# Optimization experiments

Hardware: AMD Instinct MI355X
Metric: run time of the kernel (lower is better)

## Reference

```python
import jax, jax.numpy as jnp
import numpy as np

N_NODES = 20000
DIM = 512
N_EDGES = 320000  # first N_NODES edges are self-loops so every node has a predecessor
EPS = 1e-7


def _logmap0(y):
    # Poincare ball (c=1) log map at origin: artanh(||y||) * y / ||y||
    n = jnp.linalg.norm(y, axis=-1, keepdims=True)
    nc = jnp.clip(n, EPS, 1.0 - 1e-6)
    return jnp.arctanh(nc) * y / nc


def _expmap0(v):
    # Poincare ball (c=1) exp map at origin: tanh(||v||) * v / ||v||
    n = jnp.linalg.norm(v, axis=-1, keepdims=True)
    nc = jnp.maximum(n, EPS)
    return jnp.tanh(nc) * v / nc


def setup_inputs() -> dict:
    key = jax.random.key(0)
    ks = jax.random.split(key, 9)
    x_raw = jax.random.normal(ks[0], (N_NODES, DIM), dtype=jnp.float32)
    nrm = jnp.linalg.norm(x_raw, axis=-1, keepdims=True)
    x = 0.7 * x_raw / (1.0 + nrm)  # strictly inside the unit ball

    rng = np.random.RandomState(0)
    src_rand = rng.randint(0, N_NODES, size=N_EDGES - N_NODES)
    dst_rand = rng.randint(0, N_NODES, size=N_EDGES - N_NODES)
    loop = np.arange(N_NODES)
    src = jnp.asarray(np.concatenate([loop, src_rand]), dtype=jnp.int32)
    dst = jnp.asarray(np.concatenate([loop, dst_rand]), dtype=jnp.int32)

    s = 1.0 / np.sqrt(DIM)
    Wq = jax.random.normal(ks[1], (DIM, DIM), jnp.float32) * s
    bq = jax.random.normal(ks[2], (DIM,), jnp.float32) * 0.01
    Wk = jax.random.normal(ks[3], (DIM, DIM), jnp.float32) * s
    bk = jax.random.normal(ks[4], (DIM,), jnp.float32) * 0.01
    Wv = jax.random.normal(ks[5], (DIM, DIM), jnp.float32) * s
    bv = jax.random.normal(ks[6], (DIM,), jnp.float32) * 0.01
    Wo = jax.random.normal(ks[7], (DIM, DIM), jnp.float32) * s
    bo = jax.random.normal(ks[8], (DIM,), jnp.float32) * 0.01
    return dict(x=x, src=src, dst=dst, Wq=Wq, bq=bq, Wk=Wk, bk=bk,
                Wv=Wv, bv=bv, Wo=Wo, bo=bo)


def reference(x, src, dst, Wq, bq, Wk, bk, Wv, bv, Wo, bo):
    n_nodes, d = x.shape
    scale = 1.0 / jnp.sqrt(jnp.asarray(d, x.dtype))

    t = _logmap0(x)                                  # [N, d] tangent vectors
    q = (t @ Wq.T + bq) * scale                      # torch MHA scales q
    k = t @ Wk.T + bk
    v = t @ Wv.T + bv

    # Per-destination attention over predecessor (src) neighbors.
    scores = jnp.sum(q[dst] * k[src], axis=-1)       # [E]
    m = jax.ops.segment_max(scores, dst, num_segments=n_nodes)
    e = jnp.exp(scores - m[dst])
    denom = jax.ops.segment_sum(e, dst, num_segments=n_nodes)
    alpha = e / denom[dst]                           # [E] softmax weights

    attn = jax.ops.segment_sum(alpha[:, None] * v[src], dst,
                               num_segments=n_nodes)  # [N, d]
    new_h = attn @ Wo.T + bo                          # MHA output projection
    return _expmap0(new_h)
```

## Files before the change

kernel.cpp:

```cpp
#include <hip/hip_runtime.h>
#include <math.h>
#include <stdint.h>

#define NND 20000
#define DIMK 512
#define NE  320000

typedef __attribute__((ext_vector_type(8))) short short8;
typedef __attribute__((ext_vector_type(4))) float floatx4;
typedef __attribute__((ext_vector_type(2))) float float2v;

__device__ inline float bf2f(unsigned short h) {
    unsigned int u = ((unsigned int)h) << 16;
    return __uint_as_float(u);
}
__device__ inline unsigned short f2bf(float f) {
    unsigned int u = __float_as_uint(f);
    unsigned int r = (u + 0x7fffu + ((u >> 16) & 1u)) >> 16;
    return (unsigned short)r;
}
__device__ __forceinline__ float2v bfpair(unsigned int u) {
    float2v r;
    r.x = __uint_as_float(u << 16);
    r.y = __uint_as_float(u & 0xffff0000u);
    return r;
}

__device__ __forceinline__ void gld_lds16(const unsigned short* g, unsigned short* l) {
    __builtin_amdgcn_global_load_lds(
        (const __attribute__((address_space(1))) void*)g,
        (__attribute__((address_space(3))) void*)l,
        16, 0, 0);
}

__global__ __launch_bounds__(256) void k_pre(const float* __restrict__ x,
                                             const float* __restrict__ Wq,
                                             const float* __restrict__ Wk,
                                             const float* __restrict__ Wv,
                                             const float* __restrict__ Wo,
                                             const float* __restrict__ bq,
                                             const float* __restrict__ bk,
                                             const float* __restrict__ bv,
                                             unsigned short* __restrict__ t,
                                             unsigned short* __restrict__ Wqkv,
                                             unsigned short* __restrict__ Wob,
                                             float* __restrict__ biasf,
                                             float scale_q) {
    int blk = blockIdx.x, tid = threadIdx.x;
    if (blk < 5000) {
        int row = blk * 4 + (tid >> 6);
        int lane = tid & 63;
        const floatx4* xp = (const floatx4*)(x + (size_t)row * DIMK + lane * 8);
        floatx4 x0 = xp[0], x1 = xp[1];
        float ss = 0.f;
#pragma unroll
        for (int i = 0; i < 4; i++) { ss += x0[i] * x0[i]; ss += x1[i] * x1[i]; }
#pragma unroll
        for (int off = 32; off >= 1; off >>= 1) ss += __shfl_xor(ss, off, 64);
        float n  = sqrtf(ss);
        float nc = fminf(fmaxf(n, 1e-7f), 1.0f - 1e-6f);
        float fac = atanhf(nc) / nc;
        union { short8 v; unsigned short u[8]; } o;
#pragma unroll
        for (int i = 0; i < 4; i++) { o.u[i] = f2bf(fac * x0[i]); o.u[4 + i] = f2bf(fac * x1[i]); }
        *(short8*)(t + (size_t)row * DIMK + lane * 8) = o.v;
    } else if (blk < 6024) {
        int i = (blk - 5000) * 256 + tid;
        int m = i >> 16, j = i & 65535;
        const float* in; unsigned short* out; float sc = 1.0f;
        if (m == 0)      { in = Wq; out = Wqkv;               sc = scale_q; }
        else if (m == 1) { in = Wk; out = Wqkv + 512 * DIMK;  sc = 16.0f; }
        else if (m == 2) { in = Wv; out = Wqkv + 1024 * DIMK; }
        else             { in = Wo; out = Wob; }
        floatx4 f = *(const floatx4*)(in + (size_t)j * 4);
        union { unsigned long long d; unsigned short u[4]; } o;
#pragma unroll
        for (int q = 0; q < 4; q++) o.u[q] = f2bf(f[q] * sc);
        *(unsigned long long*)(out + (size_t)j * 4) = o.d;
    } else {
        int i = (blk - 6024) * 256 + tid;
        if (i < 512) biasf[i] = bq[i] * scale_q;
        else if (i < 1024) biasf[i] = bk[i - 512] * 16.0f;
        else if (i < 1536) biasf[i] = bv[i - 1024];
    }
}

__global__ __launch_bounds__(256) void k_gemm(const unsigned short* __restrict__ A,
                                              const unsigned short* __restrict__ B,
                                              const float* __restrict__ biasf,
                                              unsigned short* __restrict__ out_q,
                                              unsigned char*  __restrict__ out_k8,
                                              unsigned short* __restrict__ out_v,
                                              float* __restrict__ out_f,
                                              int M, int MT, int NT, int Ncols) {
    __shared__ unsigned short smem[16384];
    int b = blockIdx.x;
    int xcd = b & 7, i = b >> 3;
    int nt = i % NT, mt = (i / NT) * 8 + xcd;
    if (mt >= MT) return;
    int m0 = mt * 128, n0 = nt * 128;
    int tid = threadIdx.x, wv = tid >> 6, ln = tid & 63;
    int lr = ln & 15, qd = ln >> 4;
    int mh = wv >> 1, nh = wv & 1;

    floatx4 acc[4][4] = {};
    int srow = wv * 16 + (ln >> 2);
    int scol = (ln & 3) * 8;

    {
        unsigned short* Ab = smem;
        unsigned short* Bb = smem + 8192;
#pragma unroll
        for (int p = 0; p < 2; p++) {
            int tr = p * 64 + srow;
            int ar = m0 + tr; if (ar > M - 1) ar = M - 1;
            gld_lds16(A + (size_t)ar * DIMK + scol, Ab + (p * 64 + wv * 16) * 32);
            gld_lds16(B + (size_t)(n0 + tr) * DIMK + scol, Bb + (p * 64 + wv * 16) * 32);
        }
    }

    for (int it = 0; it < 16; it++) {
        int cur = it & 1, nxt = cur ^ 1;
        __syncthreads();
        if (it + 1 < 16) {
            int kb = (it + 1) * 32;
            unsigned short* Ab = smem + nxt * 4096;
            unsigned short* Bb = smem + 8192 + nxt * 4096;
#pragma unroll
            for (int p = 0; p < 2; p++) {
                int tr = p * 64 + srow;
                int ar = m0 + tr; if (ar > M - 1) ar = M - 1;
                gld_lds16(A + (size_t)ar * DIMK + kb + scol, Ab + (p * 64 + wv * 16) * 32);
                gld_lds16(B + (size_t)(n0 + tr) * DIMK + kb + scol, Bb + (p * 64 + wv * 16) * 32);
            }
        }
        const unsigned short* Ac = smem + cur * 4096;
        const unsigned short* Bc = smem + 8192 + cur * 4096;
        short8 af[4], bfr[4];
#pragma unroll
        for (int mi = 0; mi < 4; mi++)
            af[mi] = *(const short8*)(Ac + (mh * 64 + mi * 16 + lr) * 32 + qd * 8);
#pragma unroll
        for (int ni = 0; ni < 4; ni++)
            bfr[ni] = *(const short8*)(Bc + (nh * 64 + ni * 16 + lr) * 32 + qd * 8);
#pragma unroll
        for (int mi = 0; mi < 4; mi++)
#pragma unroll
            for (int ni = 0; ni < 4; ni++)
                acc[mi][ni] = __builtin_amdgcn_mfma_f32_16x16x32_bf16(af[mi], bfr[ni], acc[mi][ni], 0, 0, 0);
    }

    float bb[4];
#pragma unroll
    for (int ni = 0; ni < 4; ni++) bb[ni] = biasf[n0 + nh * 64 + ni * 16 + lr];

    if (!out_f) {
        int region = nt >> 2;
        int col0 = (nt & 3) * 128;
        unsigned short* cs = smem;
#pragma unroll
        for (int g = 0; g < 4; g++) {
            __syncthreads();
            if (mh == (g >> 1)) {
                int miB = (g & 1) * 2;
#pragma unroll
                for (int m2 = 0; m2 < 2; m2++) {
                    int mi = miB + m2;
                    int lrow = mi * 16 + qd * 4 - (g & 1) * 32;
#pragma unroll
                    for (int ni = 0; ni < 4; ni++) {
                        int col = nh * 64 + ni * 16 + lr;
#pragma unroll
                        for (int r = 0; r < 4; r++)
                            cs[(lrow + r) * 128 + col] = f2bf(acc[mi][ni][r] + bb[ni]);
                    }
                }
            }
            __syncthreads();
#pragma unroll
            for (int itr = 0; itr < 2; itr++) {
                int slot = itr * 256 + tid;
                int row = slot >> 4, cg = slot & 15;
                int gm = m0 + g * 32 + row;
                if (gm < M) {
                    short8 vv = *(const short8*)(cs + row * 128 + cg * 8);
                    if (region == 1) {
                        union { short8 v; unsigned short u[8]; } pk; pk.v = vv;
                        int w0 = 0, w1 = 0;
                        w0 = __builtin_amdgcn_cvt_pk_fp8_f32(bf2f(pk.u[0]), bf2f(pk.u[1]), w0, false);
                        w0 = __builtin_amdgcn_cvt_pk_fp8_f32(bf2f(pk.u[2]), bf2f(pk.u[3]), w0, true);
                        w1 = __builtin_amdgcn_cvt_pk_fp8_f32(bf2f(pk.u[4]), bf2f(pk.u[5]), w1, false);
                        w1 = __builtin_amdgcn_cvt_pk_fp8_f32(bf2f(pk.u[6]), bf2f(pk.u[7]), w1, true);
                        uint2 o; o.x = (unsigned int)w0; o.y = (unsigned int)w1;
                        *(uint2*)(out_k8 + (size_t)gm * 512 + col0 + cg * 8) = o;
                    } else {
                        unsigned short* dp = (region == 0) ? out_q : out_v;
                        *(short8*)(dp + (size_t)gm * 512 + col0 + cg * 8) = vv;
                    }
                }
            }
        }
    } else {
#pragma unroll
        for (int ni = 0; ni < 4; ni++) {
            int gn = n0 + nh * 64 + ni * 16 + lr;
#pragma unroll
            for (int mi = 0; mi < 4; mi++) {
                int gm0 = m0 + mh * 64 + mi * 16 + qd * 4;
#pragma unroll
                for (int r = 0; r < 4; r++) {
                    int gm = gm0 + r;
                    if (gm < M) out_f[(size_t)gm * Ncols + gn] = acc[mi][ni][r] + bb[ni];
                }
            }
        }
    }
}

__global__ void k_hist(const int* __restrict__ dst, int* __restrict__ counts) {
    int e = blockIdx.x * 256 + threadIdx.x;
    if (e < NE) atomicAdd(&counts[dst[e]], 1);
}

__global__ __launch_bounds__(1024) void k_scan(const int* __restrict__ counts,
                                               int* __restrict__ offsets,
                                               int* __restrict__ pos) {
    const int C = 20;
    __shared__ int wsum[16];
    __shared__ int wpre[16];
    int tid = threadIdx.x, lane = tid & 63, w = tid >> 6;
    int local[C];
    int run = 0;
#pragma unroll
    for (int i = 0; i < C; i++) {
        int idx = tid * C + i;
        int c = (idx < NND) ? counts[idx] : 0;
        local[i] = run; run += c;
    }
    int v = run;
#pragma unroll
    for (int off = 1; off < 64; off <<= 1) {
        int u = __shfl_up(v, off, 64);
        if (lane >= off) v += u;
    }
    if (lane == 63) wsum[w] = v;
    __syncthreads();
    if (tid == 0) { int acc = 0; for (int i = 0; i < 16; i++) { wpre[i] = acc; acc += wsum[i]; } }
    __syncthreads();
    int texcl = wpre[w] + (v - run);
#pragma unroll
    for (int i = 0; i < C; i++) {
        int idx = tid * C + i;
        if (idx < NND) { int o = texcl + local[i]; offsets[idx] = o; pos[idx] = o; }
    }
    if (tid == 1023) offsets[NND] = texcl + run;
}

__global__ void k_scatter(const int* __restrict__ dst, const int* __restrict__ src,
                          int* __restrict__ pos, int* __restrict__ ssrc) {
    int e = blockIdx.x * 256 + threadIdx.x;
    if (e < NE) { int p = atomicAdd(&pos[dst[e]], 1); ssrc[p] = src[e]; }
}

__global__ __launch_bounds__(256) void k_fsa(const int* __restrict__ offsets,
                                             const int* __restrict__ ssrc,
                                             const unsigned short* __restrict__ qb,
                                             const unsigned char* __restrict__ kf8,
                                             const unsigned short* __restrict__ vb,
                                             unsigned short* __restrict__ attn) {
    __shared__ float sacc[4][512];
    __shared__ float sden[4];
    int n = blockIdx.x, tid = threadIdx.x, wv = tid >> 6, ln = tid & 63;
    int beg = offsets[n], end = offsets[n + 1];
    union { short8 v; unsigned short u[8]; } qu;
    qu.v = *(const short8*)(qb + (size_t)n * 512 + ln * 8);
    float2v qf2[4];
#pragma unroll
    for (int j = 0; j < 4; j++) {
        qf2[j].x = bf2f(qu.u[2 * j]);
        qf2[j].y = bf2f(qu.u[2 * j + 1]);
    }
    float2v av2[4] = {{0,0},{0,0},{0,0},{0,0}};
    float den = 0.f;
    int i = beg + wv * 2;
    for (; i + 1 < end; i += 8) {
        int s0 = ssrc[i], s1 = ssrc[i + 1];
        uint2 kd0 = *(const uint2*)(kf8 + (size_t)s0 * 512 + ln * 8);
        uint2 kd1 = *(const uint2*)(kf8 + (size_t)s1 * 512 + ln * 8);
        float2v a0 = {0, 0}, a1 = {0, 0};
        float2v p;
        p = __builtin_amdgcn_cvt_pk_f32_fp8(kd0.x, false); a0 += qf2[0] * p;
        p = __builtin_amdgcn_cvt_pk_f32_fp8(kd0.x, true);  a0 += qf2[1] * p;
        p = __builtin_amdgcn_cvt_pk_f32_fp8(kd0.y, false); a0 += qf2[2] * p;
        p = __builtin_amdgcn_cvt_pk_f32_fp8(kd0.y, true);  a0 += qf2[3] * p;
        p = __builtin_amdgcn_cvt_pk_f32_fp8(kd1.x, false); a1 += qf2[0] * p;
        p = __builtin_amdgcn_cvt_pk_f32_fp8(kd1.x, true);  a1 += qf2[1] * p;
        p = __builtin_amdgcn_cvt_pk_f32_fp8(kd1.y, false); a1 += qf2[2] * p;
        p = __builtin_amdgcn_cvt_pk_f32_fp8(kd1.y, true);  a1 += qf2[3] * p;
        float d0 = a0.x + a0.y, d1 = a1.x + a1.y;
#pragma unroll
        for (int off = 32; off >= 1; off >>= 1) {
            d0 += __shfl_xor(d0, off, 64);
            d1 += __shfl_xor(d1, off, 64);
        }
        float w0 = __expf(d0), w1 = __expf(d1);
        den += w0 + w1;
        uint4 vd0 = *(const uint4*)(vb + (size_t)s0 * 512 + ln * 8);
        uint4 vd1 = *(const uint4*)(vb + (size_t)s1 * 512 + ln * 8);
        float2v w20 = {w0, w0}, w21 = {w1, w1};
        av2[0] += w20 * bfpair(vd0.x); av2[0] += w21 * bfpair(vd1.x);
        av2[1] += w20 * bfpair(vd0.y); av2[1] += w21 * bfpair(vd1.y);
        av2[2] += w20 * bfpair(vd0.z); av2[2] += w21 * bfpair(vd1.z);
        av2[3] += w20 * bfpair(vd0.w); av2[3] += w21 * bfpair(vd1.w);
    }
    if (i < end) {
        int s0 = ssrc[i];
        uint2 kd0 = *(const uint2*)(kf8 + (size_t)s0 * 512 + ln * 8);
        float2v a0 = {0, 0};
        float2v p;
        p = __builtin_amdgcn_cvt_pk_f32_fp8(kd0.x, false); a0 += qf2[0] * p;
        p = __builtin_amdgcn_cvt_pk_f32_fp8(kd0.x, true);  a0 += qf2[1] * p;
        p = __builtin_amdgcn_cvt_pk_f32_fp8(kd0.y, false); a0 += qf2[2] * p;
        p = __builtin_amdgcn_cvt_pk_f32_fp8(kd0.y, true);  a0 += qf2[3] * p;
        float d0 = a0.x + a0.y;
#pragma unroll
        for (int off = 32; off >= 1; off >>= 1) d0 += __shfl_xor(d0, off, 64);
        float w0 = __expf(d0);
        den += w0;
        uint4 vd0 = *(const uint4*)(vb + (size_t)s0 * 512 + ln * 8);
        float2v w20 = {w0, w0};
        av2[0] += w20 * bfpair(vd0.x);
        av2[1] += w20 * bfpair(vd0.y);
        av2[2] += w20 * bfpair(vd0.z);
        av2[3] += w20 * bfpair(vd0.w);
    }
    floatx4 s0v = {av2[0].x, av2[0].y, av2[1].x, av2[1].y};
    floatx4 s1v = {av2[2].x, av2[2].y, av2[3].x, av2[3].y};
    *(floatx4*)&sacc[wv][ln * 8]     = s0v;
    *(floatx4*)&sacc[wv][ln * 8 + 4] = s1v;
    if (ln == 0) sden[wv] = den;
    __syncthreads();
    float inv = 1.0f / (sden[0] + sden[1] + sden[2] + sden[3]);
    int c = tid * 2;
    float t0 = sacc[0][c] + sacc[1][c] + sacc[2][c] + sacc[3][c];
    float t1 = sacc[0][c + 1] + sacc[1][c + 1] + sacc[2][c + 1] + sacc[3][c + 1];
    attn[(size_t)n * 512 + c]     = f2bf(t0 * inv);
    attn[(size_t)n * 512 + c + 1] = f2bf(t1 * inv);
}

__global__ __launch_bounds__(64) void k_expmap(float* h) {
    int row = blockIdx.x, lane = threadIdx.x;
    floatx4* hp = (floatx4*)(h + (size_t)row * DIMK + lane * 8);
    floatx4 h0 = hp[0], h1 = hp[1];
    float ss = 0.f;
#pragma unroll
    for (int i = 0; i < 4; i++) { ss += h0[i] * h0[i]; ss += h1[i] * h1[i]; }
#pragma unroll
    for (int off = 32; off >= 1; off >>= 1) ss += __shfl_xor(ss, off, 64);
    float n  = sqrtf(ss);
    float nc = fmaxf(n, 1e-7f);
    float fac = tanhf(nc) / nc;
#pragma unroll
    for (int i = 0; i < 4; i++) { h0[i] *= fac; h1[i] *= fac; }
    hp[0] = h0; hp[1] = h1;
}

extern "C" void kernel_launch(void* const* d_in, const int* in_sizes, int n_in,
                              void* d_out, int out_size, void* d_ws, size_t ws_size,
                              hipStream_t stream) {
    const float* x  = (const float*)d_in[0];
    const int* src  = (const int*)d_in[1];
    const int* dst  = (const int*)d_in[2];
    const float* Wq = (const float*)d_in[3];
    const float* bq = (const float*)d_in[4];
    const float* Wk = (const float*)d_in[5];
    const float* bk = (const float*)d_in[6];
    const float* Wv = (const float*)d_in[7];
    const float* bv = (const float*)d_in[8];
    const float* Wo = (const float*)d_in[9];
    const float* bo = (const float*)d_in[10];
    float* out = (float*)d_out;

    char* ws = (char*)d_ws;
    const size_t RB = (size_t)NND * DIMK * 2;
    const size_t KB8 = (size_t)NND * DIMK;
    const size_t WB = (size_t)DIMK * DIMK * 2;
    unsigned short* t    = (unsigned short*)(ws);
    unsigned short* qb   = (unsigned short*)(ws + RB);
    unsigned short* vb   = (unsigned short*)(ws + 2 * RB);
    unsigned char*  kf8  = (unsigned char*)(ws + 3 * RB);
    unsigned short* Wqkv = (unsigned short*)(ws + 3 * RB + KB8);
    unsigned short* Wob  = (unsigned short*)(ws + 3 * RB + KB8 + 3 * WB);
    float* biasf         = (float*)(ws + 3 * RB + KB8 + 4 * WB);
    char* p = ws + 3 * RB + KB8 + 4 * WB + 1536 * 4;
    int* ssrc    = (int*)p;
    int* counts  = ssrc + NE;
    int* offsets = counts + NND;
    int* pos     = offsets + NND + 2;
    unsigned short* attn = t;

    hipMemsetAsync(counts, 0, (size_t)NND * 4, stream);

    const float scale_q = 0.04419417382415922f / 16.0f;
    k_pre<<<6030, 256, 0, stream>>>(x, Wq, Wk, Wv, Wo, bq, bk, bv,
                                    t, Wqkv, Wob, biasf, scale_q);

    k_hist<<<(NE + 255) / 256, 256, 0, stream>>>(dst, counts);
    k_scan<<<1, 1024, 0, stream>>>(counts, offsets, pos);
    k_scatter<<<(NE + 255) / 256, 256, 0, stream>>>(dst, src, pos, ssrc);

    k_gemm<<<8 * 20 * 12, 256, 0, stream>>>(t, Wqkv, biasf, qb, kf8, vb, nullptr,
                                            NND, 157, 12, 1536);

    k_fsa<<<NND, 256, 0, stream>>>(offsets, ssrc, qb, kf8, vb, attn);

    k_gemm<<<8 * 20 * 4, 256, 0, stream>>>(attn, Wob, bo, nullptr, nullptr, nullptr, out,
                                           NND, 157, 4, 512);
    k_expmap<<<NND, 64, 0, stream>>>(out);
}
```

Baseline: 312.4 us.

## Store V as FP8 interleaved with K and fold histogram into prep kernel

V is now scaled by 16 and stored in FP8 next to K in one interleaved 1024-byte row per node, so each gathered neighbor's K and V come from a single row. This halves V gather traffic in the attention kernel and improves locality. The 16x scale is undone in the softmax normalisation. The degree histogram is merged into the preprocessing kernel to remove one launch. The cost is lower V precision, with FP8 rounding error in the output.

```diff
diff --git a/kernel.cpp b/kernel.cpp
--- a/kernel.cpp
+++ b/kernel.cpp
@@ -18,12 +18,6 @@
     unsigned int u = __float_as_uint(f);
     unsigned int r = (u + 0x7fffu + ((u >> 16) & 1u)) >> 16;
     return (unsigned short)r;
-}
-__device__ __forceinline__ float2v bfpair(unsigned int u) {
-    float2v r;
-    r.x = __uint_as_float(u << 16);
-    r.y = __uint_as_float(u & 0xffff0000u);
-    return r;
 }
 
 __device__ __forceinline__ void gld_lds16(const unsigned short* g, unsigned short* l) {
@@ -41,6 +35,8 @@
                                              const float* __restrict__ bq,
                                              const float* __restrict__ bk,
                                              const float* __restrict__ bv,
+                                             const int* __restrict__ dst,
+                                             int* __restrict__ counts,
                                              unsigned short* __restrict__ t,
                                              unsigned short* __restrict__ Wqkv,
                                              unsigned short* __restrict__ Wob,
@@ -70,18 +66,21 @@
         const float* in; unsigned short* out; float sc = 1.0f;
         if (m == 0)      { in = Wq; out = Wqkv;               sc = scale_q; }
         else if (m == 1) { in = Wk; out = Wqkv + 512 * DIMK;  sc = 16.0f; }
-        else if (m == 2) { in = Wv; out = Wqkv + 1024 * DIMK; }
+        else if (m == 2) { in = Wv; out = Wqkv + 1024 * DIMK; sc = 16.0f; }
         else             { in = Wo; out = Wob; }
         floatx4 f = *(const floatx4*)(in + (size_t)j * 4);
         union { unsigned long long d; unsigned short u[4]; } o;
 #pragma unroll
         for (int q = 0; q < 4; q++) o.u[q] = f2bf(f[q] * sc);
         *(unsigned long long*)(out + (size_t)j * 4) = o.d;
-    } else {
+    } else if (blk < 6030) {
         int i = (blk - 6024) * 256 + tid;
         if (i < 512) biasf[i] = bq[i] * scale_q;
         else if (i < 1024) biasf[i] = bk[i - 512] * 16.0f;
-        else if (i < 1536) biasf[i] = bv[i - 1024];
+        else if (i < 1536) biasf[i] = bv[i - 1024] * 16.0f;
+    } else {
+        int e = (blk - 6030) * 256 + tid;
+        if (e < NE) atomicAdd(&counts[dst[e]], 1);
     }
 }
 
@@ -89,8 +88,7 @@
                                               const unsigned short* __restrict__ B,
                                               const float* __restrict__ biasf,
                                               unsigned short* __restrict__ out_q,
-                                              unsigned char*  __restrict__ out_k8,
-                                              unsigned short* __restrict__ out_v,
+                                              unsigned char*  __restrict__ out_kv8,
                                               float* __restrict__ out_f,
                                               int M, int MT, int NT, int Ncols) {
     __shared__ unsigned short smem[16384];
@@ -184,7 +182,9 @@
                 int gm = m0 + g * 32 + row;
                 if (gm < M) {
                     short8 vv = *(const short8*)(cs + row * 128 + cg * 8);
-                    if (region == 1) {
+                    if (region == 0) {
+                        *(short8*)(out_q + (size_t)gm * 512 + col0 + cg * 8) = vv;
+                    } else {
                         union { short8 v; unsigned short u[8]; } pk; pk.v = vv;
                         int w0 = 0, w1 = 0;
                         w0 = __builtin_amdgcn_cvt_pk_fp8_f32(bf2f(pk.u[0]), bf2f(pk.u[1]), w0, false);
@@ -192,10 +192,8 @@
                         w1 = __builtin_amdgcn_cvt_pk_fp8_f32(bf2f(pk.u[4]), bf2f(pk.u[5]), w1, false);
                         w1 = __builtin_amdgcn_cvt_pk_fp8_f32(bf2f(pk.u[6]), bf2f(pk.u[7]), w1, true);
                         uint2 o; o.x = (unsigned int)w0; o.y = (unsigned int)w1;
-                        *(uint2*)(out_k8 + (size_t)gm * 512 + col0 + cg * 8) = o;
-                    } else {
-                        unsigned short* dp = (region == 0) ? out_q : out_v;
-                        *(short8*)(dp + (size_t)gm * 512 + col0 + cg * 8) = vv;
+                        size_t off = (size_t)gm * 1024 + (region == 2 ? 512 : 0) + col0 + cg * 8;
+                        *(uint2*)(out_kv8 + off) = o;
                     }
                 }
             }
@@ -215,11 +213,6 @@
             }
         }
     }
-}
-
-__global__ void k_hist(const int* __restrict__ dst, int* __restrict__ counts) {
-    int e = blockIdx.x * 256 + threadIdx.x;
-    if (e < NE) atomicAdd(&counts[dst[e]], 1);
 }
 
 __global__ __launch_bounds__(1024) void k_scan(const int* __restrict__ counts,
@@ -265,8 +258,7 @@
 __global__ __launch_bounds__(256) void k_fsa(const int* __restrict__ offsets,
                                              const int* __restrict__ ssrc,
                                              const unsigned short* __restrict__ qb,
-                                             const unsigned char* __restrict__ kf8,
-                                             const unsigned short* __restrict__ vb,
+                                             const unsigned char* __restrict__ kv8,
                                              unsigned short* __restrict__ attn) {
     __shared__ float sacc[4][512];
     __shared__ float sden[4];
@@ -284,9 +276,10 @@
     float den = 0.f;
     int i = beg + wv * 2;
     for (; i + 1 < end; i += 8) {
-        int s0 = ssrc[i], s1 = ssrc[i + 1];
-        uint2 kd0 = *(const uint2*)(kf8 + (size_t)s0 * 512 + ln * 8);
-        uint2 kd1 = *(const uint2*)(kf8 + (size_t)s1 * 512 + ln * 8);
+        const unsigned char* p0 = kv8 + (size_t)ssrc[i] * 1024 + ln * 8;
+        const unsigned char* p1 = kv8 + (size_t)ssrc[i + 1] * 1024 + ln * 8;
+        uint2 kd0 = *(const uint2*)p0;
+        uint2 kd1 = *(const uint2*)p1;
         float2v a0 = {0, 0}, a1 = {0, 0};
         float2v p;
         p = __builtin_amdgcn_cvt_pk_f32_fp8(kd0.x, false); a0 += qf2[0] * p;
@@ -305,17 +298,21 @@
         }
         float w0 = __expf(d0), w1 = __expf(d1);
         den += w0 + w1;
-        uint4 vd0 = *(const uint4*)(vb + (size_t)s0 * 512 + ln * 8);
-        uint4 vd1 = *(const uint4*)(vb + (size_t)s1 * 512 + ln * 8);
+        uint2 vd0 = *(const uint2*)(p0 + 512);
+        uint2 vd1 = *(const uint2*)(p1 + 512);
         float2v w20 = {w0, w0}, w21 = {w1, w1};
-        av2[0] += w20 * bfpair(vd0.x); av2[0] += w21 * bfpair(vd1.x);
-        av2[1] += w20 * bfpair(vd0.y); av2[1] += w21 * bfpair(vd1.y);
-        av2[2] += w20 * bfpair(vd0.z); av2[2] += w21 * bfpair(vd1.z);
-        av2[3] += w20 * bfpair(vd0.w); av2[3] += w21 * bfpair(vd1.w);
+        p = __builtin_amdgcn_cvt_pk_f32_fp8(vd0.x, false); av2[0] += w20 * p;
+        p = __builtin_amdgcn_cvt_pk_f32_fp8(vd0.x, true);  av2[1] += w20 * p;
+        p = __builtin_amdgcn_cvt_pk_f32_fp8(vd0.y, false); av2[2] += w20 * p;
+        p = __builtin_amdgcn_cvt_pk_f32_fp8(vd0.y, true);  av2[3] += w20 * p;
+        p = __builtin_amdgcn_cvt_pk_f32_fp8(vd1.x, false); av2[0] += w21 * p;
+        p = __builtin_amdgcn_cvt_pk_f32_fp8(vd1.x, true);  av2[1] += w21 * p;
+        p = __builtin_amdgcn_cvt_pk_f32_fp8(vd1.y, false); av2[2] += w21 * p;
+        p = __builtin_amdgcn_cvt_pk_f32_fp8(vd1.y, true);  av2[3] += w21 * p;
     }
     if (i < end) {
-        int s0 = ssrc[i];
-        uint2 kd0 = *(const uint2*)(kf8 + (size_t)s0 * 512 + ln * 8);
+        const unsigned char* p0 = kv8 + (size_t)ssrc[i] * 1024 + ln * 8;
+        uint2 kd0 = *(const uint2*)p0;
         float2v a0 = {0, 0};
         float2v p;
         p = __builtin_amdgcn_cvt_pk_f32_fp8(kd0.x, false); a0 += qf2[0] * p;
@@ -327,12 +324,12 @@
         for (int off = 32; off >= 1; off >>= 1) d0 += __shfl_xor(d0, off, 64);
         float w0 = __expf(d0);
         den += w0;
-        uint4 vd0 = *(const uint4*)(vb + (size_t)s0 * 512 + ln * 8);
+        uint2 vd0 = *(const uint2*)(p0 + 512);
         float2v w20 = {w0, w0};
-        av2[0] += w20 * bfpair(vd0.x);
-        av2[1] += w20 * bfpair(vd0.y);
-        av2[2] += w20 * bfpair(vd0.z);
-        av2[3] += w20 * bfpair(vd0.w);
+        p = __builtin_amdgcn_cvt_pk_f32_fp8(vd0.x, false); av2[0] += w20 * p;
+        p = __builtin_amdgcn_cvt_pk_f32_fp8(vd0.x, true);  av2[1] += w20 * p;
+        p = __builtin_amdgcn_cvt_pk_f32_fp8(vd0.y, false); av2[2] += w20 * p;
+        p = __builtin_amdgcn_cvt_pk_f32_fp8(vd0.y, true);  av2[3] += w20 * p;
     }
     floatx4 s0v = {av2[0].x, av2[0].y, av2[1].x, av2[1].y};
     floatx4 s1v = {av2[2].x, av2[2].y, av2[3].x, av2[3].y};
@@ -340,7 +337,7 @@
     *(floatx4*)&sacc[wv][ln * 8 + 4] = s1v;
     if (ln == 0) sden[wv] = den;
     __syncthreads();
-    float inv = 1.0f / (sden[0] + sden[1] + sden[2] + sden[3]);
+    float inv = 0.0625f / (sden[0] + sden[1] + sden[2] + sden[3]);
     int c = tid * 2;
     float t0 = sacc[0][c] + sacc[1][c] + sacc[2][c] + sacc[3][c];
     float t1 = sacc[0][c + 1] + sacc[1][c + 1] + sacc[2][c + 1] + sacc[3][c + 1];
@@ -383,16 +380,15 @@
 
     char* ws = (char*)d_ws;
     const size_t RB = (size_t)NND * DIMK * 2;
-    const size_t KB8 = (size_t)NND * DIMK;
+    const size_t KVB = (size_t)NND * 1024;
     const size_t WB = (size_t)DIMK * DIMK * 2;
     unsigned short* t    = (unsigned short*)(ws);
     unsigned short* qb   = (unsigned short*)(ws + RB);
-    unsigned short* vb   = (unsigned short*)(ws + 2 * RB);
-    unsigned char*  kf8  = (unsigned char*)(ws + 3 * RB);
-    unsigned short* Wqkv = (unsigned short*)(ws + 3 * RB + KB8);
-    unsigned short* Wob  = (unsigned short*)(ws + 3 * RB + KB8 + 3 * WB);
-    float* biasf         = (float*)(ws + 3 * RB + KB8 + 4 * WB);
-    char* p = ws + 3 * RB + KB8 + 4 * WB + 1536 * 4;
+    unsigned char*  kv8  = (unsigned char*)(ws + 2 * RB);
+    unsigned short* Wqkv = (unsigned short*)(ws + 2 * RB + KVB);
+    unsigned short* Wob  = (unsigned short*)(ws + 2 * RB + KVB + 3 * WB);
+    float* biasf         = (float*)(ws + 2 * RB + KVB + 4 * WB);
+    char* p = ws + 2 * RB + KVB + 4 * WB + 1536 * 4;
     int* ssrc    = (int*)p;
     int* counts  = ssrc + NE;
     int* offsets = counts + NND;
@@ -402,19 +398,18 @@
     hipMemsetAsync(counts, 0, (size_t)NND * 4, stream);
 
     const float scale_q = 0.04419417382415922f / 16.0f;
-    k_pre<<<6030, 256, 0, stream>>>(x, Wq, Wk, Wv, Wo, bq, bk, bv,
+    k_pre<<<7280, 256, 0, stream>>>(x, Wq, Wk, Wv, Wo, bq, bk, bv, dst, counts,
                                     t, Wqkv, Wob, biasf, scale_q);
 
-    k_hist<<<(NE + 255) / 256, 256, 0, stream>>>(dst, counts);
     k_scan<<<1, 1024, 0, stream>>>(counts, offsets, pos);
     k_scatter<<<(NE + 255) / 256, 256, 0, stream>>>(dst, src, pos, ssrc);
 
-    k_gemm<<<8 * 20 * 12, 256, 0, stream>>>(t, Wqkv, biasf, qb, kf8, vb, nullptr,
+    k_gemm<<<8 * 20 * 12, 256, 0, stream>>>(t, Wqkv, biasf, qb, kv8, nullptr,
                                             NND, 157, 12, 1536);
 
-    k_fsa<<<NND, 256, 0, stream>>>(offsets, ssrc, qb, kf8, vb, attn);
-
-    k_gemm<<<8 * 20 * 4, 256, 0, stream>>>(attn, Wob, bo, nullptr, nullptr, nullptr, out,
+    k_fsa<<<NND, 256, 0, stream>>>(offsets, ssrc, qb, kv8, attn);
+
+    k_gemm<<<8 * 20 * 4, 256, 0, stream>>>(attn, Wob, bo, nullptr, nullptr, out,
                                            NND, 157, 4, 512);
     k_expmap<<<NND, 64, 0, stream>>>(out);
 }
```

Measured after the change: 293.5 us. 1.06x faster.
